# Optimization experiments

Hardware: AMD Instinct MI355X
Metric: run time of the kernel (lower is better)

Reference implementation:

```python
import jax, jax.numpy as jnp
import numpy as np
from jax import lax

B, T, H, F, K, NB, MAXLEN = 32, 1024, 384, 384, 3, 256, 2048


def _ln(x, g, b, eps=1e-5):
    m = jnp.mean(x, axis=-1, keepdims=True)
    v = jnp.var(x, axis=-1, keepdims=True)
    return (x - m) * lax.rsqrt(v + eps) * g + b


def _conv(x, w, b):
    # x: (B, T, Cin), w: (K, Cin, Cout); SAME padding == torch padding=(K-1)//2 for K=3, stride 1
    y = lax.conv_general_dilated(x, w, (1,), 'SAME', dimension_numbers=('NWC', 'WIO', 'NWC'))
    return y + b


def _predictor(x, mask, w1, b1, g1, be1, w2, b2, g2, be2, wo, bo):
    h = _ln(jax.nn.relu(_conv(x, w1, b1)), g1, be1)
    h = _ln(jax.nn.relu(_conv(h, w2, b2)), g2, be2)
    out = jnp.einsum('btf,f->bt', h, wo) + bo  # Linear(F -> 1).squeeze(-1)
    return jnp.where(mask, 0.0, out)


def _length_regulate(x, dur, max_len):
    # vectorized equivalent of torch per-sample expand+cat+pad
    csum = jnp.cumsum(dur, axis=1)                      # (B, T)
    total = csum[:, -1]                                 # (B,) = mel_len
    frames = jnp.arange(max_len)                        # (M,)
    # frame f belongs to phoneme i with csum[i-1] <= f < csum[i]
    idx = jax.vmap(lambda c: jnp.searchsorted(c, frames, side='right'))(csum)  # (B, M)
    idx = jnp.clip(idx, 0, x.shape[1] - 1)
    out = jnp.take_along_axis(x, idx[:, :, None], axis=1)                      # (B, M, H)
    valid = (frames[None, :] < total[:, None]).astype(x.dtype)                 # zero-pad tail
    return out * valid[:, :, None], total


def setup_inputs() -> dict:
    key = jax.random.key(0)
    ks = iter(jax.random.split(key, 64))
    nk = lambda: next(ks)
    d = {}
    d['x'] = jax.random.normal(nk(), (B, T, H), jnp.float32)
    d['src_mask'] = jnp.zeros((B, T), jnp.bool_)
    d['duration'] = jax.random.randint(nk(), (B, T), 0, 4)
    d['max_len'] = MAXLEN
    for p in ('dp', 'pp', 'ep'):
        d[p + '_w1'] = jax.random.normal(nk(), (K, H, F), jnp.float32) * 0.02
        d[p + '_b1'] = jnp.zeros((F,), jnp.float32)
        d[p + '_g1'] = jnp.ones((F,), jnp.float32)
        d[p + '_be1'] = jnp.zeros((F,), jnp.float32)
        d[p + '_w2'] = jax.random.normal(nk(), (K, F, F), jnp.float32) * 0.02
        d[p + '_b2'] = jnp.zeros((F,), jnp.float32)
        d[p + '_g2'] = jnp.ones((F,), jnp.float32)
        d[p + '_be2'] = jnp.zeros((F,), jnp.float32)
        d[p + '_wo'] = jax.random.normal(nk(), (F,), jnp.float32) * 0.02
        d[p + '_bo'] = jnp.zeros((1,), jnp.float32)
    d['pitch_bins'] = jnp.linspace(0.0, 1.0, NB - 1, dtype=jnp.float32)
    d['energy_bins'] = jnp.linspace(0.0, 1.0, NB - 1, dtype=jnp.float32)
    d['pitch_emb'] = jax.random.normal(nk(), (NB, H), jnp.float32) * 0.02
    d['energy_emb'] = jax.random.normal(nk(), (NB, H), jnp.float32) * 0.02
    d['pitch_target'] = jax.random.uniform(nk(), (B, T), jnp.float32)
    d['energy_target'] = jax.random.uniform(nk(), (B, T), jnp.float32)
    return d


def reference(x, src_mask, duration, max_len,
              dp_w1, dp_b1, dp_g1, dp_be1, dp_w2, dp_b2, dp_g2, dp_be2, dp_wo, dp_bo,
              pp_w1, pp_b1, pp_g1, pp_be1, pp_w2, pp_b2, pp_g2, pp_be2, pp_wo, pp_bo,
              ep_w1, ep_b1, ep_g1, ep_be1, ep_w2, ep_b2, ep_g2, ep_be2, ep_wo, ep_bo,
              pitch_bins, energy_bins, pitch_emb, energy_emb, pitch_target, energy_target):
    log_dur = _predictor(x, src_mask, dp_w1, dp_b1, dp_g1, dp_be1, dp_w2, dp_b2, dp_g2, dp_be2, dp_wo, dp_bo)
    # phoneme-level pitch (target path: bucketize target, torch.bucketize right=False == searchsorted left)
    pitch_pred = _predictor(x, src_mask, pp_w1, pp_b1, pp_g1, pp_be1, pp_w2, pp_b2, pp_g2, pp_be2, pp_wo, pp_bo)
    x = x + pitch_emb[jnp.searchsorted(pitch_bins, pitch_target, side='left')]
    # phoneme-level energy (predictor sees x AFTER pitch embedding add, as in torch)
    energy_pred = _predictor(x, src_mask, ep_w1, ep_b1, ep_g1, ep_be1, ep_w2, ep_b2, ep_g2, ep_be2, ep_wo, ep_bo)
    x = x + energy_emb[jnp.searchsorted(energy_bins, energy_target, side='left')]
    x_out, mel_len = _length_regulate(x, duration, max_len)
    return (x_out, pitch_pred, energy_pred, log_dur, mel_len)
```

## Files before the change

### kernel.cpp

```cpp
#include <hip/hip_runtime.h>

#define B_ 32
#define T_ 1024
#define C_ 384
#define MAXLEN_ 2048
#define NBINS_ 255
#define WPK1 442368
#define BTC  (32 * 1024 * 384)

typedef __attribute__((ext_vector_type(8))) short short8v;
typedef __attribute__((ext_vector_type(4))) float floatx4;

__device__ __forceinline__ unsigned short f2bf(float f) {
    unsigned u = __float_as_uint(f);
    u += 0x7fffu + ((u >> 16) & 1u);
    return (unsigned short)(u >> 16);
}
__device__ __forceinline__ float bf2f(unsigned short h) {
    return __uint_as_float(((unsigned)h) << 16);
}

struct CvP {
    const unsigned short* xin;
    size_t xin_stride;
    const unsigned short* wpk;
    const float* bias[3];
    const float* gamma[3];
    const float* beta[3];
    const float* wo[3];
    const float* bo[3];
    unsigned short* hout;
    float* pred[3];
    const float* pbins;
    const float* pemb;
    const float* ptgt;
    int final_flag;
};

#define ARS 392

__global__ __launch_bounds__(512, 2) void conv_mfma3(CvP P)
{
    __shared__ unsigned short As[130 * ARS];
    __shared__ float rsum[8][64];
    __shared__ float rsq[8][64];

    const int tid  = threadIdx.x;
    const int wave = tid >> 6;
    const int wg   = wave >> 2;
    const int wv   = wave & 3;
    const int lane = tid & 63;
    const int lq   = lane >> 4;
    const int ln   = lane & 15;
    const int p    = blockIdx.x >> 8;
    const int bi   = blockIdx.x & 255;
    const int b    = bi >> 3;
    const int t0   = (bi & 7) << 7;
    const int nb   = wv * 96;

    const unsigned short* xin = P.xin + (size_t)p * P.xin_stride;
    const bool fuse_emb = (!P.final_flag) && (p == 2);

    for (int i = tid; i < 130 * 48; i += 512) {
        const int row = i / 48;
        const int c   = i - row * 48;
        const int t   = t0 - 1 + row;
        short8v v = (short8v){0,0,0,0,0,0,0,0};
        if ((unsigned)t < (unsigned)T_) {
            v = *(const short8v*)(xin + ((size_t)(b << 10) + t) * C_ + c * 8);
            if (fuse_emb) {
                const float tg = P.ptgt[(b << 10) + t];
                int lo = 0, hi = NBINS_;
                while (lo < hi) {
                    const int mid = (lo + hi) >> 1;
                    if (P.pbins[mid] < tg) lo = mid + 1; else hi = mid;
                }
                const float* er = P.pemb + (size_t)lo * C_ + c * 8;
#pragma unroll
                for (int j = 0; j < 8; ++j) {
                    const float f = bf2f((unsigned short)v[j]) + er[j];
                    v[j] = (short)f2bf(f);
                }
            }
        }
        *(short8v*)&As[row * ARS + c * 8] = v;
    }
    __syncthreads();

    floatx4 acc[24];
#pragma unroll
    for (int i = 0; i < 24; ++i) acc[i] = (floatx4){0.f, 0.f, 0.f, 0.f};

    const unsigned short* bbase =
        P.wpk + (size_t)p * WPK1 + ((size_t)(nb + ln) << 5) + (lq << 3);

    short8v bA[6], bB[6];
#pragma unroll
    for (int nt = 0; nt < 6; ++nt) {
        bA[nt] = *(const short8v*)(bbase + (nt << 9));
        bB[nt] = *(const short8v*)(bbase + 12288 + (nt << 9));
    }

    int kc = 0, hb = 0;
    for (int r = 0; r < 36; r += 2) {
        {
            short8v afrag[4];
#pragma unroll
            for (int mt = 0; mt < 4; ++mt)
                afrag[mt] = *(const short8v*)
                    &As[(wg * 64 + mt * 16 + ln + kc) * ARS + hb + (lq << 3)];
#pragma unroll
            for (int mt = 0; mt < 4; ++mt)
#pragma unroll
                for (int nt = 0; nt < 6; ++nt)
                    acc[mt * 6 + nt] = __builtin_amdgcn_mfma_f32_16x16x32_bf16(
                        afrag[mt], bA[nt], acc[mt * 6 + nt], 0, 0, 0);
            if (r + 2 < 36) {
                const unsigned short* np_ = bbase + (size_t)(r + 2) * 12288;
#pragma unroll
                for (int nt = 0; nt < 6; ++nt)
                    bA[nt] = *(const short8v*)(np_ + (nt << 9));
            }
            hb += 32; if (hb == 384) { hb = 0; ++kc; }
        }
        {
            short8v afrag[4];
#pragma unroll
            for (int mt = 0; mt < 4; ++mt)
                afrag[mt] = *(const short8v*)
                    &As[(wg * 64 + mt * 16 + ln + kc) * ARS + hb + (lq << 3)];
#pragma unroll
            for (int mt = 0; mt < 4; ++mt)
#pragma unroll
                for (int nt = 0; nt < 6; ++nt)
                    acc[mt * 6 + nt] = __builtin_amdgcn_mfma_f32_16x16x32_bf16(
                        afrag[mt], bB[nt], acc[mt * 6 + nt], 0, 0, 0);
            if (r + 3 < 36) {
                const unsigned short* np_ = bbase + (size_t)(r + 3) * 12288;
#pragma unroll
                for (int nt = 0; nt < 6; ++nt)
                    bB[nt] = *(const short8v*)(np_ + (nt << 9));
            }
            hb += 32; if (hb == 384) { hb = 0; ++kc; }
        }
    }

    float bcol[6], gcol[6], becol[6], wcol[6];
#pragma unroll
    for (int nt = 0; nt < 6; ++nt) {
        const int col = nb + nt * 16 + ln;
        bcol[nt]  = P.bias[p][col];
        gcol[nt]  = P.gamma[p][col];
        becol[nt] = P.beta[p][col];
        wcol[nt]  = P.final_flag ? P.wo[p][col] : 0.f;
    }

#pragma unroll
    for (int mt = 0; mt < 4; ++mt) {
#pragma unroll
        for (int rg = 0; rg < 4; ++rg) {
            float s = 0.f, q = 0.f;
#pragma unroll
            for (int nt = 0; nt < 6; ++nt) {
                float v = acc[mt * 6 + nt][rg] + bcol[nt];
                v = v > 0.f ? v : 0.f;
                acc[mt * 6 + nt][rg] = v;
                s += v; q += v * v;
            }
#pragma unroll
            for (int off = 1; off < 16; off <<= 1) {
                s += __shfl_xor(s, off, 64);
                q += __shfl_xor(q, off, 64);
            }
            if (ln == mt * 4 + rg) {
                rsum[wave][mt * 16 + lq * 4 + rg] = s;
                rsq [wave][mt * 16 + lq * 4 + rg] = q;
            }
        }
    }
    __syncthreads();

    float mean_[16], rstd_[16];
#pragma unroll
    for (int mt = 0; mt < 4; ++mt) {
#pragma unroll
        for (int rg = 0; rg < 4; ++rg) {
            const int row = mt * 16 + lq * 4 + rg;
            const int wb  = wg << 2;
            const float s = rsum[wb][row] + rsum[wb+1][row] + rsum[wb+2][row] + rsum[wb+3][row];
            const float q = rsq[wb][row] + rsq[wb+1][row] + rsq[wb+2][row] + rsq[wb+3][row];
            const float m = s * (1.f / 384.f);
            const float var = q * (1.f / 384.f) - m * m;
            mean_[mt * 4 + rg] = m;
            rstd_[mt * 4 + rg] = rsqrtf(var + 1e-5f);
        }
    }

    if (!P.final_flag) {
        unsigned short* hout = P.hout + (size_t)p * BTC;
#pragma unroll
        for (int mt = 0; mt < 4; ++mt)
#pragma unroll
            for (int rg = 0; rg < 4; ++rg) {
                const float m = mean_[mt * 4 + rg], rs = rstd_[mt * 4 + rg];
                const int grow = (bi << 7) + wg * 64 + mt * 16 + lq * 4 + rg;
#pragma unroll
                for (int nt = 0; nt < 6; ++nt) {
                    const float v = (acc[mt * 6 + nt][rg] - m) * rs * gcol[nt] + becol[nt];
                    hout[((size_t)b << 10) * 0 + (size_t)grow * C_ + nb + nt * 16 + ln] = f2bf(v);
                }
            }
    } else {
        __syncthreads();
#pragma unroll
        for (int mt = 0; mt < 4; ++mt) {
#pragma unroll
            for (int rg = 0; rg < 4; ++rg) {
                const float m = mean_[mt * 4 + rg], rs = rstd_[mt * 4 + rg];
                float pr = 0.f;
#pragma unroll
                for (int nt = 0; nt < 6; ++nt)
                    pr += ((acc[mt * 6 + nt][rg] - m) * rs * gcol[nt] + becol[nt]) * wcol[nt];
#pragma unroll
                for (int off = 1; off < 16; off <<= 1)
                    pr += __shfl_xor(pr, off, 64);
                if (ln == mt * 4 + rg)
                    rsum[wave][mt * 16 + lq * 4 + rg] = pr;
            }
        }
        __syncthreads();
        if (tid < 128) {
            const int half = tid >> 6, r_ = tid & 63, wb = half << 2;
            P.pred[p][(bi << 7) + tid] =
                rsum[wb][r_] + rsum[wb+1][r_] + rsum[wb+2][r_] + rsum[wb+3][r_] + P.bo[p][0];
        }
    }
}

__global__ __launch_bounds__(256) void cast_x_kernel(
    const float* __restrict__ src, unsigned short* __restrict__ dst)
{
    const int i = blockIdx.x * 256 + threadIdx.x;
    const float4 v = *(const float4*)(src + (size_t)i * 4);
    ushort4 o;
    o.x = f2bf(v.x); o.y = f2bf(v.y); o.z = f2bf(v.z); o.w = f2bf(v.w);
    *(ushort4*)(dst + (size_t)i * 4) = o;
}

__global__ __launch_bounds__(256) void pack_w_kernel(
    const float* __restrict__ s0, const float* __restrict__ s1,
    const float* __restrict__ s2, const float* __restrict__ s3,
    const float* __restrict__ s4, const float* __restrict__ s5,
    unsigned short* __restrict__ dst)
{
    const int wsel = blockIdx.y;
    const float* src = wsel == 0 ? s0 : wsel == 1 ? s1 : wsel == 2 ? s2
                     : wsel == 3 ? s3 : wsel == 4 ? s4 : s5;
    const int o = blockIdx.x * 256 + threadIdx.x;
    const int r = o >> 14;
    const int rem = o & 12287;
    const int n = rem >> 5;
    const int k = rem & 31;
    dst[(size_t)wsel * WPK1 + o] = f2bf(src[(size_t)(r * 32 + k) * C_ + n]);
}

__global__ __launch_bounds__(256) void cumsum_kernel(
    const int* __restrict__ dur, int* __restrict__ csum,
    float* __restrict__ mel_len)
{
    __shared__ int part[256];
    const int b = blockIdx.x;
    const int tid = threadIdx.x;
    int l[4];
    int s = 0;
#pragma unroll
    for (int i = 0; i < 4; ++i) { l[i] = dur[b * T_ + tid * 4 + i]; s += l[i]; }
    part[tid] = s;
    __syncthreads();
    for (int off = 1; off < 256; off <<= 1) {
        int u = 0;
        if (tid >= off) u = part[tid - off];
        __syncthreads();
        part[tid] += u;
        __syncthreads();
    }
    const int incl = part[tid];
    int run = incl - s;
#pragma unroll
    for (int i = 0; i < 4; ++i) {
        run += l[i];
        csum[b * T_ + tid * 4 + i] = run;
    }
    if (tid == 255) mel_len[b] = (float)incl;
}

__global__ __launch_bounds__(256) void length_reg_kernel(
    const float* __restrict__ x, const int* __restrict__ csum,
    const float* __restrict__ pbins, const float* __restrict__ pemb,
    const float* __restrict__ ptgt,
    const float* __restrict__ ebins, const float* __restrict__ eemb,
    const float* __restrict__ etgt,
    float* __restrict__ out)
{
    const int g    = blockIdx.x * 256 + threadIdx.x;
    const int c4   = g % 96;
    const int rest = g / 96;
    const int frame = rest & (MAXLEN_ - 1);
    const int b     = rest >> 11;
    const int* cr = csum + (b << 10);
    const int total = cr[T_ - 1];
    float4 v = make_float4(0.f, 0.f, 0.f, 0.f);
    if (frame < total) {
        int lo = 0, hi = T_;
        while (lo < hi) {
            const int mid = (lo + hi) >> 1;
            if (cr[mid] <= frame) lo = mid + 1; else hi = mid;
        }
        const int t = lo > T_ - 1 ? T_ - 1 : lo;
        const int row = (b << 10) + t;
        v = *(const float4*)(x + (size_t)row * C_ + c4 * 4);
        const float ptg = ptgt[row];
        int plo = 0, phi = NBINS_;
        while (plo < phi) {
            const int mid = (plo + phi) >> 1;
            if (pbins[mid] < ptg) plo = mid + 1; else phi = mid;
        }
        const float etg = etgt[row];
        int elo = 0, ehi = NBINS_;
        while (elo < ehi) {
            const int mid = (elo + ehi) >> 1;
            if (ebins[mid] < etg) elo = mid + 1; else ehi = mid;
        }
        const float4 pe = *(const float4*)(pemb + (size_t)plo * C_ + c4 * 4);
        const float4 ee = *(const float4*)(eemb + (size_t)elo * C_ + c4 * 4);
        v.x += pe.x + ee.x; v.y += pe.y + ee.y;
        v.z += pe.z + ee.z; v.w += pe.w + ee.w;
    }
    *(float4*)(out + (size_t)g * 4) = v;
}

extern "C" void kernel_launch(void* const* d_in, const int* in_sizes, int n_in,
                              void* d_out, int out_size, void* d_ws, size_t ws_size,
                              hipStream_t stream)
{
    const float* x        = (const float*)d_in[0];
    const int*   duration = (const int*)d_in[2];
    const float* P[3][10];
    for (int p = 0; p < 3; ++p)
        for (int q = 0; q < 10; ++q)
            P[p][q] = (const float*)d_in[4 + p * 10 + q];
    const float* pitch_bins    = (const float*)d_in[34];
    const float* energy_bins   = (const float*)d_in[35];
    const float* pitch_emb     = (const float*)d_in[36];
    const float* energy_emb    = (const float*)d_in[37];
    const float* pitch_target  = (const float*)d_in[38];
    const float* energy_target = (const float*)d_in[39];

    float* out_x      = (float*)d_out;
    float* out_pitch  = out_x + (size_t)B_ * MAXLEN_ * C_;
    float* out_energy = out_pitch + B_ * T_;
    float* out_logdur = out_energy + B_ * T_;
    float* out_mellen = out_logdur + B_ * T_;

    unsigned short* xbf = (unsigned short*)out_x;
    unsigned short* h1b = xbf + (size_t)BTC;

    unsigned short* wpk = (unsigned short*)d_ws;
    int* csum = (int*)(wpk + (size_t)6 * WPK1);

    const dim3 blk(256);

    cast_x_kernel<<<12288, blk, 0, stream>>>(x, xbf);
    pack_w_kernel<<<dim3(1728, 6), blk, 0, stream>>>(
        P[0][0], P[0][4], P[1][0], P[1][4], P[2][0], P[2][4], wpk);

    CvP P1;
    P1.xin = xbf; P1.xin_stride = 0; P1.wpk = wpk;
    for (int p = 0; p < 3; ++p) {
        P1.bias[p]  = P[p][1];
        P1.gamma[p] = P[p][2];
        P1.beta[p]  = P[p][3];
        P1.wo[p]    = nullptr;
        P1.bo[p]    = nullptr;
        P1.pred[p]  = nullptr;
    }
    P1.hout = h1b;
    P1.pbins = pitch_bins; P1.pemb = pitch_emb; P1.ptgt = pitch_target;
    P1.final_flag = 0;

    CvP P2;
    P2.xin = h1b; P2.xin_stride = BTC; P2.wpk = wpk + (size_t)3 * WPK1;
    for (int p = 0; p < 3; ++p) {
        P2.bias[p]  = P[p][5];
        P2.gamma[p] = P[p][6];
        P2.beta[p]  = P[p][7];
        P2.wo[p]    = P[p][8];
        P2.bo[p]    = P[p][9];
    }
    P2.pred[0] = out_logdur; P2.pred[1] = out_pitch; P2.pred[2] = out_energy;
    P2.hout = nullptr;
    P2.pbins = nullptr; P2.pemb = nullptr; P2.ptgt = nullptr;
    P2.final_flag = 1;

    conv_mfma3<<<768, dim3(512), 0, stream>>>(P1);
    conv_mfma3<<<768, dim3(512), 0, stream>>>(P2);

    cumsum_kernel<<<B_, blk, 0, stream>>>(duration, csum, out_mellen);
    length_reg_kernel<<<24576, blk, 0, stream>>>(
        x, csum, pitch_bins, pitch_emb, pitch_target,
        energy_bins, energy_emb, energy_target, out_x);
}
```

Baseline: 543.9 us.

## Fuse fp32-to-bf16 cast into conv load, halve tiles, coalesce weight packing

Removes the separate cast_x kernel: the first conv stage now reads the fp32 input directly and converts it to bf16 while filling shared memory, which avoids writing and re-reading a bf16 copy of x. Blocks shrink from 512 threads covering 128 rows to 256 threads covering 64 rows, doubling the grid and cutting the LDS tile to roughly half. The LN reduction buffers now reuse the A-tile LDS, which needs an extra barrier. Weights are repacked into lane-contiguous order so each wave's B fragment loads are fully coalesced. In exchange, each block loads a larger halo relative to its rows, and the fp32 reads double the input bytes fetched per block.

```diff
diff --git a/kernel.cpp b/kernel.cpp
--- a/kernel.cpp
+++ b/kernel.cpp
@@ -7,6 +7,7 @@
 #define NBINS_ 255
 #define WPK1 442368
 #define BTC  (32 * 1024 * 384)
+#define ARS 392
 
 typedef __attribute__((ext_vector_type(8))) short short8v;
 typedef __attribute__((ext_vector_type(4))) float floatx4;
@@ -16,13 +17,10 @@
     u += 0x7fffu + ((u >> 16) & 1u);
     return (unsigned short)(u >> 16);
 }
-__device__ __forceinline__ float bf2f(unsigned short h) {
-    return __uint_as_float(((unsigned)h) << 16);
-}
 
 struct CvP {
-    const unsigned short* xin;
-    size_t xin_stride;
+    const float* xf;
+    const unsigned short* xb;
     const unsigned short* wpk;
     const float* bias[3];
     const float* gamma[3];
@@ -37,63 +35,25 @@
     int final_flag;
 };
 
-#define ARS 392
-
-__global__ __launch_bounds__(512, 2) void conv_mfma3(CvP P)
+__global__ __launch_bounds__(256, 2) void conv_mfma3(CvP P)
 {
-    __shared__ unsigned short As[130 * ARS];
-    __shared__ float rsum[8][64];
-    __shared__ float rsq[8][64];
+    __shared__ unsigned short As[66 * ARS];
+    float* rsum = (float*)As;
+    float* rsq  = rsum + 256;
 
     const int tid  = threadIdx.x;
     const int wave = tid >> 6;
-    const int wg   = wave >> 2;
-    const int wv   = wave & 3;
     const int lane = tid & 63;
     const int lq   = lane >> 4;
     const int ln   = lane & 15;
-    const int p    = blockIdx.x >> 8;
-    const int bi   = blockIdx.x & 255;
-    const int b    = bi >> 3;
-    const int t0   = (bi & 7) << 7;
-    const int nb   = wv * 96;
-
-    const unsigned short* xin = P.xin + (size_t)p * P.xin_stride;
-    const bool fuse_emb = (!P.final_flag) && (p == 2);
-
-    for (int i = tid; i < 130 * 48; i += 512) {
-        const int row = i / 48;
-        const int c   = i - row * 48;
-        const int t   = t0 - 1 + row;
-        short8v v = (short8v){0,0,0,0,0,0,0,0};
-        if ((unsigned)t < (unsigned)T_) {
-            v = *(const short8v*)(xin + ((size_t)(b << 10) + t) * C_ + c * 8);
-            if (fuse_emb) {
-                const float tg = P.ptgt[(b << 10) + t];
-                int lo = 0, hi = NBINS_;
-                while (lo < hi) {
-                    const int mid = (lo + hi) >> 1;
-                    if (P.pbins[mid] < tg) lo = mid + 1; else hi = mid;
-                }
-                const float* er = P.pemb + (size_t)lo * C_ + c * 8;
-#pragma unroll
-                for (int j = 0; j < 8; ++j) {
-                    const float f = bf2f((unsigned short)v[j]) + er[j];
-                    v[j] = (short)f2bf(f);
-                }
-            }
-        }
-        *(short8v*)&As[row * ARS + c * 8] = v;
-    }
-    __syncthreads();
-
-    floatx4 acc[24];
-#pragma unroll
-    for (int i = 0; i < 24; ++i) acc[i] = (floatx4){0.f, 0.f, 0.f, 0.f};
+    const int p    = blockIdx.x >> 9;
+    const int bi   = blockIdx.x & 511;
+    const int b    = bi >> 4;
+    const int t0   = (bi & 15) << 6;
+    const int nb   = wave * 96;
 
     const unsigned short* bbase =
-        P.wpk + (size_t)p * WPK1 + ((size_t)(nb + ln) << 5) + (lq << 3);
-
+        P.wpk + (size_t)p * WPK1 + wave * 3072 + (size_t)lane * 8;
     short8v bA[6], bB[6];
 #pragma unroll
     for (int nt = 0; nt < 6; ++nt) {
@@ -101,49 +61,101 @@
         bB[nt] = *(const short8v*)(bbase + 12288 + (nt << 9));
     }
 
-    int kc = 0, hb = 0;
-    for (int r = 0; r < 36; r += 2) {
-        {
-            short8v afrag[4];
-#pragma unroll
-            for (int mt = 0; mt < 4; ++mt)
-                afrag[mt] = *(const short8v*)
-                    &As[(wg * 64 + mt * 16 + ln + kc) * ARS + hb + (lq << 3)];
-#pragma unroll
-            for (int mt = 0; mt < 4; ++mt)
-#pragma unroll
-                for (int nt = 0; nt < 6; ++nt)
-                    acc[mt * 6 + nt] = __builtin_amdgcn_mfma_f32_16x16x32_bf16(
-                        afrag[mt], bA[nt], acc[mt * 6 + nt], 0, 0, 0);
-            if (r + 2 < 36) {
-                const unsigned short* np_ = bbase + (size_t)(r + 2) * 12288;
-#pragma unroll
-                for (int nt = 0; nt < 6; ++nt)
-                    bA[nt] = *(const short8v*)(np_ + (nt << 9));
-            }
-            hb += 32; if (hb == 384) { hb = 0; ++kc; }
-        }
-        {
-            short8v afrag[4];
-#pragma unroll
-            for (int mt = 0; mt < 4; ++mt)
-                afrag[mt] = *(const short8v*)
-                    &As[(wg * 64 + mt * 16 + ln + kc) * ARS + hb + (lq << 3)];
-#pragma unroll
-            for (int mt = 0; mt < 4; ++mt)
-#pragma unroll
-                for (int nt = 0; nt < 6; ++nt)
-                    acc[mt * 6 + nt] = __builtin_amdgcn_mfma_f32_16x16x32_bf16(
-                        afrag[mt], bB[nt], acc[mt * 6 + nt], 0, 0, 0);
-            if (r + 3 < 36) {
-                const unsigned short* np_ = bbase + (size_t)(r + 3) * 12288;
-#pragma unroll
-                for (int nt = 0; nt < 6; ++nt)
-                    bB[nt] = *(const short8v*)(np_ + (nt << 9));
-            }
-            hb += 32; if (hb == 384) { hb = 0; ++kc; }
-        }
-    }
+    if (!P.final_flag) {
+        const bool fuse_emb = (p == 2);
+        for (int i = tid; i < 66 * 48; i += 256) {
+            const int row = i / 48;
+            const int c   = i - row * 48;
+            const int t   = t0 - 1 + row;
+            short8v v = (short8v){0,0,0,0,0,0,0,0};
+            if ((unsigned)t < (unsigned)T_) {
+                const float* sp = P.xf + ((size_t)(b << 10) + t) * C_ + c * 8;
+                float f[8];
+                *(float4*)&f[0] = *(const float4*)sp;
+                *(float4*)&f[4] = *(const float4*)(sp + 4);
+                if (fuse_emb) {
+                    const float tg = P.ptgt[(b << 10) + t];
+                    int lo = 0, hi = NBINS_;
+                    while (lo < hi) {
+                        const int mid = (lo + hi) >> 1;
+                        if (P.pbins[mid] < tg) lo = mid + 1; else hi = mid;
+                    }
+                    const float* er = P.pemb + (size_t)lo * C_ + c * 8;
+#pragma unroll
+                    for (int j = 0; j < 8; ++j) f[j] += er[j];
+                }
+#pragma unroll
+                for (int j = 0; j < 8; ++j) v[j] = (short)f2bf(f[j]);
+            }
+            *(short8v*)&As[row * ARS + c * 8] = v;
+        }
+    } else {
+        const unsigned short* xb = P.xb + (size_t)p * BTC;
+        for (int i = tid; i < 66 * 48; i += 256) {
+            const int row = i / 48;
+            const int c   = i - row * 48;
+            const int t   = t0 - 1 + row;
+            short8v v = (short8v){0,0,0,0,0,0,0,0};
+            if ((unsigned)t < (unsigned)T_)
+                v = *(const short8v*)(xb + ((size_t)(b << 10) + t) * C_ + c * 8);
+            *(short8v*)&As[row * ARS + c * 8] = v;
+        }
+    }
+    __syncthreads();
+
+    floatx4 acc[24];
+#pragma unroll
+    for (int i = 0; i < 24; ++i) acc[i] = (floatx4){0.f, 0.f, 0.f, 0.f};
+
+    const unsigned short* abase = &As[ln * ARS + lq * 8];
+    const unsigned short* bpA = bbase + 2 * 12288;
+    const unsigned short* bpB = bbase + 3 * 12288;
+
+#pragma unroll
+    for (int kc = 0; kc < 3; ++kc) {
+#pragma unroll
+        for (int h2 = 0; h2 < 6; ++h2) {
+            const int hb = h2 * 64;
+            const int r  = kc * 12 + h2 * 2;
+            {
+                short8v afrag[4];
+#pragma unroll
+                for (int mt = 0; mt < 4; ++mt)
+                    afrag[mt] = *(const short8v*)(abase + (mt * 16 + kc) * ARS + hb);
+#pragma unroll
+                for (int mt = 0; mt < 4; ++mt)
+#pragma unroll
+                    for (int nt = 0; nt < 6; ++nt)
+                        acc[mt * 6 + nt] = __builtin_amdgcn_mfma_f32_16x16x32_bf16(
+                            afrag[mt], bA[nt], acc[mt * 6 + nt], 0, 0, 0);
+                if (r + 2 < 36) {
+#pragma unroll
+                    for (int nt = 0; nt < 6; ++nt)
+                        bA[nt] = *(const short8v*)(bpA + (nt << 9));
+                    bpA += 24576;
+                }
+            }
+            {
+                short8v afrag[4];
+#pragma unroll
+                for (int mt = 0; mt < 4; ++mt)
+                    afrag[mt] = *(const short8v*)(abase + (mt * 16 + kc) * ARS + hb + 32);
+#pragma unroll
+                for (int mt = 0; mt < 4; ++mt)
+#pragma unroll
+                    for (int nt = 0; nt < 6; ++nt)
+                        acc[mt * 6 + nt] = __builtin_amdgcn_mfma_f32_16x16x32_bf16(
+                            afrag[mt], bB[nt], acc[mt * 6 + nt], 0, 0, 0);
+                if (r + 3 < 36) {
+#pragma unroll
+                    for (int nt = 0; nt < 6; ++nt)
+                        bB[nt] = *(const short8v*)(bpB + (nt << 9));
+                    bpB += 24576;
+                }
+            }
+        }
+    }
+    __syncthreads();
 
     float bcol[6], gcol[6], becol[6], wcol[6];
 #pragma unroll
@@ -173,8 +185,8 @@
                 q += __shfl_xor(q, off, 64);
             }
             if (ln == mt * 4 + rg) {
-                rsum[wave][mt * 16 + lq * 4 + rg] = s;
-                rsq [wave][mt * 16 + lq * 4 + rg] = q;
+                rsum[wave * 64 + mt * 16 + lq * 4 + rg] = s;
+                rsq [wave * 64 + mt * 16 + lq * 4 + rg] = q;
             }
         }
     }
@@ -186,9 +198,8 @@
 #pragma unroll
         for (int rg = 0; rg < 4; ++rg) {
             const int row = mt * 16 + lq * 4 + rg;
-            const int wb  = wg << 2;
-            const float s = rsum[wb][row] + rsum[wb+1][row] + rsum[wb+2][row] + rsum[wb+3][row];
-            const float q = rsq[wb][row] + rsq[wb+1][row] + rsq[wb+2][row] + rsq[wb+3][row];
+            const float s = rsum[row] + rsum[64 + row] + rsum[128 + row] + rsum[192 + row];
+            const float q = rsq[row] + rsq[64 + row] + rsq[128 + row] + rsq[192 + row];
             const float m = s * (1.f / 384.f);
             const float var = q * (1.f / 384.f) - m * m;
             mean_[mt * 4 + rg] = m;
@@ -203,11 +214,11 @@
 #pragma unroll
             for (int rg = 0; rg < 4; ++rg) {
                 const float m = mean_[mt * 4 + rg], rs = rstd_[mt * 4 + rg];
-                const int grow = (bi << 7) + wg * 64 + mt * 16 + lq * 4 + rg;
+                const int grow = (bi << 6) + mt * 16 + lq * 4 + rg;
 #pragma unroll
                 for (int nt = 0; nt < 6; ++nt) {
                     const float v = (acc[mt * 6 + nt][rg] - m) * rs * gcol[nt] + becol[nt];
-                    hout[((size_t)b << 10) * 0 + (size_t)grow * C_ + nb + nt * 16 + ln] = f2bf(v);
+                    hout[(size_t)grow * C_ + nb + nt * 16 + ln] = f2bf(v);
                 }
             }
     } else {
@@ -225,26 +236,14 @@
                 for (int off = 1; off < 16; off <<= 1)
                     pr += __shfl_xor(pr, off, 64);
                 if (ln == mt * 4 + rg)
-                    rsum[wave][mt * 16 + lq * 4 + rg] = pr;
+                    rsum[wave * 64 + mt * 16 + lq * 4 + rg] = pr;
             }
         }
         __syncthreads();
-        if (tid < 128) {
-            const int half = tid >> 6, r_ = tid & 63, wb = half << 2;
-            P.pred[p][(bi << 7) + tid] =
-                rsum[wb][r_] + rsum[wb+1][r_] + rsum[wb+2][r_] + rsum[wb+3][r_] + P.bo[p][0];
-        }
-    }
-}
-
-__global__ __launch_bounds__(256) void cast_x_kernel(
-    const float* __restrict__ src, unsigned short* __restrict__ dst)
-{
-    const int i = blockIdx.x * 256 + threadIdx.x;
-    const float4 v = *(const float4*)(src + (size_t)i * 4);
-    ushort4 o;
-    o.x = f2bf(v.x); o.y = f2bf(v.y); o.z = f2bf(v.z); o.w = f2bf(v.w);
-    *(ushort4*)(dst + (size_t)i * 4) = o;
+        if (tid < 64)
+            P.pred[p][(bi << 6) + tid] =
+                rsum[tid] + rsum[64 + tid] + rsum[128 + tid] + rsum[192 + tid] + P.bo[p][0];
+    }
 }
 
 __global__ __launch_bounds__(256) void pack_w_kernel(
@@ -257,10 +256,16 @@
     const float* src = wsel == 0 ? s0 : wsel == 1 ? s1 : wsel == 2 ? s2
                      : wsel == 3 ? s3 : wsel == 4 ? s4 : s5;
     const int o = blockIdx.x * 256 + threadIdx.x;
-    const int r = o >> 14;
-    const int rem = o & 12287;
-    const int n = rem >> 5;
-    const int k = rem & 31;
+    const int r    = o / 12288;
+    const int rem  = o - r * 12288;
+    const int wv   = rem / 3072;
+    const int rem2 = rem - wv * 3072;
+    const int nt   = rem2 >> 9;
+    const int li   = rem2 & 511;
+    const int lane = li >> 3;
+    const int j    = li & 7;
+    const int n = wv * 96 + nt * 16 + (lane & 15);
+    const int k = ((lane >> 4) << 3) + j;
     dst[(size_t)wsel * WPK1 + o] = f2bf(src[(size_t)(r * 32 + k) * C_ + n]);
 }
 
@@ -362,20 +367,18 @@
     float* out_logdur = out_energy + B_ * T_;
     float* out_mellen = out_logdur + B_ * T_;
 
-    unsigned short* xbf = (unsigned short*)out_x;
-    unsigned short* h1b = xbf + (size_t)BTC;
+    unsigned short* h1b = (unsigned short*)out_x;
 
     unsigned short* wpk = (unsigned short*)d_ws;
     int* csum = (int*)(wpk + (size_t)6 * WPK1);
 
     const dim3 blk(256);
 
-    cast_x_kernel<<<12288, blk, 0, stream>>>(x, xbf);
     pack_w_kernel<<<dim3(1728, 6), blk, 0, stream>>>(
         P[0][0], P[0][4], P[1][0], P[1][4], P[2][0], P[2][4], wpk);
 
     CvP P1;
-    P1.xin = xbf; P1.xin_stride = 0; P1.wpk = wpk;
+    P1.xf = x; P1.xb = nullptr; P1.wpk = wpk;
     for (int p = 0; p < 3; ++p) {
         P1.bias[p]  = P[p][1];
         P1.gamma[p] = P[p][2];
@@ -389,7 +392,7 @@
     P1.final_flag = 0;
 
     CvP P2;
-    P2.xin = h1b; P2.xin_stride = BTC; P2.wpk = wpk + (size_t)3 * WPK1;
+    P2.xf = nullptr; P2.xb = h1b; P2.wpk = wpk + (size_t)3 * WPK1;
     for (int p = 0; p < 3; ++p) {
         P2.bias[p]  = P[p][5];
         P2.gamma[p] = P[p][6];
@@ -402,8 +405,8 @@
     P2.pbins = nullptr; P2.pemb = nullptr; P2.ptgt = nullptr;
     P2.final_flag = 1;
 
-    conv_mfma3<<<768, dim3(512), 0, stream>>>(P1);
-    conv_mfma3<<<768, dim3(512), 0, stream>>>(P2);
+    conv_mfma3<<<1536, blk, 0, stream>>>(P1);
+    conv_mfma3<<<1536, blk, 0, stream>>>(P2);
 
     cumsum_kernel<<<B_, blk, 0, stream>>>(duration, csum, out_mellen);
     length_reg_kernel<<<24576, blk, 0, stream>>>(
```

Result: faster. 502.0 us (-7.7%).
